# Performance work log

Hardware: AMD Instinct MI355X
Metric: run time of the kernel (lower is better)

Reference implementation:

```python
import jax, jax.numpy as jnp
import numpy as np

N_NODES = 100000
N_EDGES = 1600000
HIDDEN = 64
N_LAYERS = 3
N_CLASSES = 2
N_GRAPHS = 128
NEG_SLOPE = 0.2  # PyG GATConv default negative_slope


def setup_inputs() -> dict:
    key = jax.random.key(0)
    ks = jax.random.split(key, 8)
    x = jax.random.randint(ks[0], (N_NODES,), 0, 2)
    edge_index = jax.random.randint(ks[1], (2, N_EDGES), 0, N_NODES)
    batch = jnp.sort(jax.random.randint(ks[2], (N_NODES,), 0, N_GRAPHS))
    scale = 1.0 / np.sqrt(HIDDEN)
    embed_table = jax.random.normal(ks[3], (2, HIDDEN), jnp.float32)
    Ws = jax.random.normal(ks[4], (N_LAYERS, HIDDEN, HIDDEN), jnp.float32) * scale
    a_srcs = jax.random.normal(ks[5], (N_LAYERS, HIDDEN), jnp.float32) * scale
    a_dsts = jax.random.normal(ks[6], (N_LAYERS, HIDDEN), jnp.float32) * scale
    biases = jnp.zeros((N_LAYERS, HIDDEN), jnp.float32)
    W_out = jax.random.normal(ks[7], (HIDDEN, N_CLASSES), jnp.float32) * scale
    b_out = jnp.zeros((N_CLASSES,), jnp.float32)
    return {"x": x, "edge_index": edge_index, "batch": batch,
            "embed_table": embed_table, "Ws": Ws, "a_srcs": a_srcs,
            "a_dsts": a_dsts, "biases": biases, "W_out": W_out, "b_out": b_out}


def _gat_layer(h, src, dst, W, a_s, a_d, b):
    # h: [N, D]; src/dst: [E'] (self loops included) -> PyG GATConv, heads=1
    hW = h @ W                                   # [N, D]
    e = jax.nn.leaky_relu((hW @ a_s)[src] + (hW @ a_d)[dst], NEG_SLOPE)  # [E']
    m = jax.ops.segment_max(e, dst, num_segments=N_NODES)               # stable softmax per dst
    ex = jnp.exp(e - m[dst])
    denom = jax.ops.segment_sum(ex, dst, num_segments=N_NODES)
    alpha = ex / denom[dst]                      # [E']
    out = jax.ops.segment_sum(hW[src] * alpha[:, None], dst, num_segments=N_NODES)
    return out + b


def reference(x, edge_index, batch, embed_table, Ws, a_srcs, a_dsts, biases, W_out, b_out):
    loop = jnp.arange(N_NODES)
    src = jnp.concatenate([edge_index[0], loop])  # PyG add_self_loops=True
    dst = jnp.concatenate([edge_index[1], loop])
    h = embed_table[x]                            # [N, D]
    for l in range(N_LAYERS):
        h = _gat_layer(h, src, dst, Ws[l], a_srcs[l], a_dsts[l], biases[l])
        if l < N_LAYERS - 1:
            h = jax.nn.relu(h)
    sums = jax.ops.segment_sum(h, batch, num_segments=N_GRAPHS)
    counts = jax.ops.segment_sum(jnp.ones((N_NODES,), h.dtype), batch, num_segments=N_GRAPHS)
    pooled = sums / jnp.maximum(counts, 1.0)[:, None]  # global_mean_pool
    return pooled @ W_out + b_out                      # [G, num_classes]
```

## Files before the change

### kernel.cpp

```cpp
#include <hip/hip_runtime.h>
#include <hip/hip_bf16.h>
#include <float.h>

#define N_NODES 100000
#define N_EDGES 1600000
#define HIDDEN 64
#define N_GRAPHS 128
#define NEG_SLOPE 0.2f
#define ETOT (N_EDGES + N_NODES)

#define BSHIFT 9
#define NB ((N_NODES + 511) >> BSHIFT)
#define PAIR_CHUNK 4096
#define PAIR_BLOCKS ((N_EDGES + PAIR_CHUNK - 1) / PAIR_CHUNK)
#define XBIT_BLOCKS ((N_NODES + 255) / 256)
#define TBL_BLOCKS (NLVL / 4)
#define CAP 12288

#define NREP 64
#define REP_STRIDE 272
#define NLVL 512

__device__ __forceinline__ unsigned short f2bf(float f) {
    unsigned u = __float_as_uint(f);
    unsigned r = (u + 0x7FFFu + ((u >> 16) & 1u)) >> 16;
    return (unsigned short)r;
}
__device__ __forceinline__ float blo(unsigned u) { return __uint_as_float(u << 16); }
__device__ __forceinline__ float bhi(unsigned u) { return __uint_as_float(u & 0xFFFF0000u); }
__device__ __forceinline__ int sb0(unsigned u) { return (int)((unsigned)(u << 24)) >> 24; }
__device__ __forceinline__ int sb1(unsigned u) { return (int)((unsigned)(u << 16)) >> 24; }
__device__ __forceinline__ int sb2(unsigned u) { return (int)((unsigned)(u << 8)) >> 24; }
__device__ __forceinline__ int sb3(unsigned u) { return (int)u >> 24; }


__global__ __launch_bounds__(256) void k_prep(
    const int* __restrict__ x,
    const float* __restrict__ embed, const float* __restrict__ Ws,
    const float* __restrict__ biases, const float* __restrict__ a_srcs,
    const float* __restrict__ a_dsts, const float* __restrict__ W_out,
    int* __restrict__ gcnt, float* __restrict__ pool_acc,
    unsigned* __restrict__ xb,
    unsigned char* __restrict__ Tq8, float* __restrict__ Tscl,
    float* __restrict__ Ts1s, float* __restrict__ Ts1d,
    float* __restrict__ sparams)
{
    int t = threadIdx.x, b = blockIdx.x;

    if (b < TBL_BLOCKS) {
        if (b == 0 && t < NB) gcnt[t] = 0;
        if (b < NREP && t < 2 * N_GRAPHS) pool_acc[b * REP_STRIDE + t] = 0.f;

        int l = b * 4 + (t >> 6);
        int f = t & 63;
        float r0 = 0.f, r1 = 0.f;
#pragma unroll 8
        for (int k = 0; k < 64; ++k) {
            float w = Ws[k * 64 + f];
            r0 = fmaf(embed[k], w, r0);
            r1 = fmaf(embed[64 + k], w, r1);
        }
        if (l == 0) {
            float as = a_srcs[f], ad = a_dsts[f];
            float t0 = r0 * as, t1 = r1 * as, t2 = r0 * ad, t3 = r1 * ad;
#pragma unroll
            for (int off = 32; off >= 1; off >>= 1) {
                t0 += __shfl_xor(t0, off); t1 += __shfl_xor(t1, off);
                t2 += __shfl_xor(t2, off); t3 += __shfl_xor(t3, off);
            }
            if (f == 0) { sparams[0] = t0; sparams[1] = t1; sparams[2] = t2; sparams[3] = t3; }
        }
        if (l == 1) {
            float b2 = biases[128 + f];
            float t4 = b2 * W_out[f * 2];
            float t5 = b2 * W_out[f * 2 + 1];
#pragma unroll
            for (int off = 32; off >= 1; off >>= 1) {
                t4 += __shfl_xor(t4, off); t5 += __shfl_xor(t5, off);
            }
            if (f == 0) { sparams[4] = t4; sparams[5] = t5; }
        }
        float c1 = (float)l * (1.f / (NLVL - 1));
        float o = fmaxf(biases[f] + r0 + c1 * (r1 - r0), 0.f);
        const float* W1 = Ws + 4096;
        float h = 0.f;
#pragma unroll 8
        for (int k = 0; k < 64; ++k) h = fmaf(__shfl(o, k), W1[k * 64 + f], h);
        float ss = h * a_srcs[64 + f];
        float sd = h * a_dsts[64 + f];
        float am = fabsf(h);
#pragma unroll
        for (int off = 32; off >= 1; off >>= 1) {
            ss += __shfl_xor(ss, off);
            sd += __shfl_xor(sd, off);
            am = fmaxf(am, __shfl_xor(am, off));
        }
        float iscl = (am > 0.f) ? 127.f / am : 0.f;
        Tq8[l * 64 + f] = (unsigned char)(__float2int_rn(h * iscl) & 255);
        if (f == 0) { Tscl[l] = am * (1.f / 127.f); Ts1s[l] = ss; Ts1d[l] = sd; }
    } else {
        int i = (b - TBL_BLOCKS) * 256 + t;
        int lane = t & 63;
        bool bb = (i < N_NODES) && (x[i] != 0);
        unsigned long long m = __ballot(bb);
        int wid = i >> 6;
        if (i < N_NODES + 64) {
            if (lane == 0) xb[wid * 2] = (unsigned)m;
            if (lane == 32) xb[wid * 2 + 1] = (unsigned)(m >> 32);
        }
    }
}


__global__ __launch_bounds__(256) void k_scatter(
    const int* __restrict__ e0, const int* __restrict__ e1,
    const unsigned* __restrict__ xb, int* __restrict__ gcnt,
    int* __restrict__ pairs)
{
    __shared__ int hcnt[NB];
    __shared__ int base[NB];
    int t = threadIdx.x, b = blockIdx.x;
    if (t < NB) hcnt[t] = 0;
    __syncthreads();
    int ebase = b * PAIR_CHUNK;
    int ecount = min(PAIR_CHUNK, N_EDGES - ebase);
    for (int i = 4 * t; i < ecount; i += 1024) {
        int4 d4 = *(const int4*)(e1 + ebase + i);
        atomicAdd(&hcnt[d4.x >> BSHIFT], 1);
        atomicAdd(&hcnt[d4.y >> BSHIFT], 1);
        atomicAdd(&hcnt[d4.z >> BSHIFT], 1);
        atomicAdd(&hcnt[d4.w >> BSHIFT], 1);
    }
    __syncthreads();
    if (t < NB) {
        int c = hcnt[t];
        base[t] = c ? atomicAdd(&gcnt[t], c) : 0;
        hcnt[t] = 0;
    }
    __syncthreads();
    for (int i = 4 * t; i < ecount; i += 1024) {
        int4 s4 = *(const int4*)(e0 + ebase + i);
        int4 d4 = *(const int4*)(e1 + ebase + i);
        int ss[4] = {s4.x, s4.y, s4.z, s4.w};
        int dd[4] = {d4.x, d4.y, d4.z, d4.w};
#pragma unroll
        for (int j = 0; j < 4; ++j) {
            int s = ss[j], d = dd[j];
            int xv = (xb[s >> 5] >> (s & 31)) & 1;
            int B = d >> BSHIFT;
            int idx = atomicAdd(&hcnt[B], 1);
            pairs[B * CAP + base[B] + idx] = (xv << 26) | ((d & 511) << 17) | s;
        }
    }
}

__global__ __launch_bounds__(1024) void k_csr_bucket(
    const int* __restrict__ pairs, const int* __restrict__ gcnt,
    const int* __restrict__ x, const float* __restrict__ sparams,
    int* __restrict__ rowptr, int* __restrict__ col,
    unsigned short* __restrict__ cidx)
{
    __shared__ int deg[512];
    __shared__ int excl[512];
    __shared__ int cnt2[512];
    __shared__ int wsum[16];
    __shared__ int p0sh;
    int b = blockIdx.x;
    int t = threadIdx.x;
    int nb = b << BSHIFT;
    int nodes = min(512, N_NODES - nb);

    int pv = (t < b) ? gcnt[t] : 0;
#pragma unroll
    for (int off = 32; off >= 1; off >>= 1) pv += __shfl_xor(pv, off);
    if ((t & 63) == 0) wsum[t >> 6] = pv;
    __syncthreads();
    if (t == 0) {
        int s = 0;
#pragma unroll
        for (int i = 0; i < 16; ++i) s += wsum[i];
        p0sh = s;
    }

    int xself = 0;
    if (t < 512) {
        xself = (t < nodes) ? (x[nb + t] & 1) : 0;
        deg[t] = (t < nodes) ? (1 | (xself << 16)) : 0;
        cnt2[t] = 1;
    }
    __syncthreads();
    int cnt = gcnt[b];
    int pbase = b * CAP;
    for (int i = t; i < cnt; i += 1024) {
        int p = pairs[pbase + i];
        atomicAdd(&deg[(p >> 17) & 511], 1 | (((p >> 26) & 1) << 16));
    }
    __syncthreads();

    int packed = (t < 512) ? deg[t] : 0;
    int val = packed & 0xFFFF;
    int kx = packed >> 16;
    if (t < nodes) {
        float ss0 = sparams[0], ss1 = sparams[1];
        float sd = xself ? sparams[3] : sparams[2];
        float e0 = ss0 + sd; e0 = (e0 >= 0.f) ? e0 : NEG_SLOPE * e0;
        float e1 = ss1 + sd; e1 = (e1 >= 0.f) ? e1 : NEG_SLOPE * e1;
        float pp0 = __expf(e0), pp1 = __expf(e1);
        float kn = (float)kx, dn = (float)(val - kx);
        float c1 = kn * pp1 / (dn * pp0 + kn * pp1);
        cidx[nb + t] = (unsigned short)__float2int_rn(c1 * (float)(NLVL - 1));
    }

    int xx = val;
#pragma unroll
    for (int off = 1; off < 64; off <<= 1) {
        int y = __shfl_up(xx, off);
        if ((t & 63) >= off) xx += y;
    }
    if ((t & 63) == 63 && t < 512) wsum[t >> 6] = xx;
    __syncthreads();
    if (t == 0) {
        int s = 0;
#pragma unroll
        for (int i = 0; i < 8; ++i) { int v = wsum[i]; wsum[i] = s; s += v; }
    }
    __syncthreads();
    int ex = xx - val + wsum[t >> 6];
    if (t < 512) excl[t] = ex;

    int p0 = p0sh;
    int colbase = p0 + nb;
    if (t < nodes) {
        rowptr[nb + t] = colbase + ex;
        col[colbase + ex] = nb + t;
    }
    if (b == NB - 1 && t == 0) rowptr[N_NODES] = ETOT;
    __syncthreads();
    for (int i = t; i < cnt; i += 1024) {
        int p = pairs[pbase + i];
        int li = (p >> 17) & 511;
        int pos = colbase + excl[li] + atomicAdd(&cnt2[li], 1);
        col[pos] = p & 0x1FFFF;
    }
}


__global__ __launch_bounds__(256) void k_agg1(
    const unsigned char* __restrict__ Tq8, const float* __restrict__ Tscl,
    const float* __restrict__ Ts1s, const float* __restrict__ Ts1d,
    const unsigned short* __restrict__ cidx, const int* __restrict__ col,
    const int* __restrict__ rowptr, const float* __restrict__ bias,
    unsigned short* __restrict__ hout)
{
    __shared__ float2 stash[4][64];
    int t = threadIdx.x;
    int wave = t >> 6, lane = t & 63;
    int h = lane >> 5, hl = lane & 31;
    int base = blockIdx.x * 8 + wave * 2;
    if (base >= N_NODES) return;
    const char* hb = (const char*)Tq8;

    int node = base + h;
    bool valid = (node < N_NODES);
    int row = 0, end = 0;
    if (valid) { row = rowptr[node]; end = rowptr[node + 1]; }
    int deg = end - row;
    int degO = __shfl_xor(deg, 32);
    bool fast = (deg <= 32) && (degO <= 32);

    if (fast) {
        int idx = 0;
        float p = 0.f, sc = 0.f;
        if (hl < deg) idx = cidx[col[row + hl]];
        float sdi = Ts1d[__shfl(idx, h * 32)];
        if (hl < deg) {
            float ee = Ts1s[idx] + sdi;
            ee = (ee >= 0.f) ? ee : NEG_SLOPE * ee;
            p = __expf(ee);
            sc = Tscl[idx];
        }
        stash[wave][lane] = make_float2(p * sc, __int_as_float(idx * 64));

        int q = hl >> 4;
        int f = hl & 15;
        int f4 = f * 4;
        int sb = h * 32;
        float a0 = 0.f, a1 = 0.f, a2 = 0.f, a3 = 0.f;
        int degr = (deg + 7) & ~7;
        for (int j = q; j < degr; j += 8) {
            float2 e0 = stash[wave][sb + j];
            float2 e1 = stash[wave][sb + j + 2];
            float2 e2 = stash[wave][sb + j + 4];
            float2 e3 = stash[wave][sb + j + 6];
            unsigned v0 = *(const unsigned*)(hb + (__float_as_int(e0.y) + f4));
            unsigned v1 = *(const unsigned*)(hb + (__float_as_int(e1.y) + f4));
            unsigned v2 = *(const unsigned*)(hb + (__float_as_int(e2.y) + f4));
            unsigned v3 = *(const unsigned*)(hb + (__float_as_int(e3.y) + f4));
            a0 = fmaf(e0.x, (float)sb0(v0), a0);
            a1 = fmaf(e0.x, (float)sb1(v0), a1);
            a2 = fmaf(e0.x, (float)sb2(v0), a2);
            a3 = fmaf(e0.x, (float)sb3(v0), a3);
            a0 = fmaf(e1.x, (float)sb0(v1), a0);
            a1 = fmaf(e1.x, (float)sb1(v1), a1);
            a2 = fmaf(e1.x, (float)sb2(v1), a2);
            a3 = fmaf(e1.x, (float)sb3(v1), a3);
            a0 = fmaf(e2.x, (float)sb0(v2), a0);
            a1 = fmaf(e2.x, (float)sb1(v2), a1);
            a2 = fmaf(e2.x, (float)sb2(v2), a2);
            a3 = fmaf(e2.x, (float)sb3(v2), a3);
            a0 = fmaf(e3.x, (float)sb0(v3), a0);
            a1 = fmaf(e3.x, (float)sb1(v3), a1);
            a2 = fmaf(e3.x, (float)sb2(v3), a2);
            a3 = fmaf(e3.x, (float)sb3(v3), a3);
        }
        float denom = p;
#pragma unroll
        for (int off = 16; off >= 1; off >>= 1) denom += __shfl_xor(denom, off);
        float inv = 1.f / denom;
        a0 += __shfl_xor(a0, 16);
        a1 += __shfl_xor(a1, 16);
        a2 += __shfl_xor(a2, 16);
        a3 += __shfl_xor(a3, 16);
        if (hl < 16 && valid) {
            float4 bb = *(const float4*)&bias[4 * f];
            ushort4 pk;
            pk.x = f2bf(fmaxf(fmaf(a0, inv, bb.x), 0.f));
            pk.y = f2bf(fmaxf(fmaf(a1, inv, bb.y), 0.f));
            pk.z = f2bf(fmaxf(fmaf(a2, inv, bb.z), 0.f));
            pk.w = f2bf(fmaxf(fmaf(a3, inv, bb.w), 0.f));
            *(ushort4*)&hout[node * 64 + 4 * f] = pk;
        }
    } else {
        for (int s = 0; s < 2; ++s) {
            int nd = base + s;
            if (nd >= N_NODES) continue;
            int r = rowptr[nd], e = rowptr[nd + 1];
            float sdi = Ts1d[cidx[nd]];
            float m = -FLT_MAX;
            for (int j = r + lane; j < e; j += 64) {
                float ee = Ts1s[cidx[col[j]]] + sdi;
                ee = (ee >= 0.f) ? ee : NEG_SLOPE * ee;
                m = fmaxf(m, ee);
            }
#pragma unroll
            for (int off = 32; off >= 1; off >>= 1) m = fmaxf(m, __shfl_xor(m, off));
            float denom = 0.f;
            for (int j = r + lane; j < e; j += 64) {
                float ee = Ts1s[cidx[col[j]]] + sdi;
                ee = (ee >= 0.f) ? ee : NEG_SLOPE * ee;
                denom += __expf(ee - m);
            }
#pragma unroll
            for (int off = 32; off >= 1; off >>= 1) denom += __shfl_xor(denom, off);
            float inv = 1.f / denom;
            float acc = 0.f;
            for (int j = r; j < e; ++j) {
                int idxj = cidx[col[j]];
                float ee = Ts1s[idxj] + sdi;
                ee = (ee >= 0.f) ? ee : NEG_SLOPE * ee;
                float w = __expf(ee - m) * inv * Tscl[idxj];
                int bq = (int)(signed char)Tq8[idxj * 64 + lane];
                acc = fmaf(w, (float)bq, acc);
            }
            hout[nd * 64 + lane] = f2bf(fmaxf(acc + bias[lane], 0.f));
        }
    }
}


__global__ __launch_bounds__(256) void k_gemm2(
    const unsigned* __restrict__ h32, const float* __restrict__ W,
    const float* __restrict__ a_s, const float* __restrict__ a_d,
    const float* __restrict__ W_out,
    float2* __restrict__ z2, float* __restrict__ s_src, float* __restrict__ s_dst)
{
    __shared__ float Wl[64 * 64];
    __shared__ float hT[64 * 68];
    int t = threadIdx.x;
    int r0 = blockIdx.x * 64;

    for (int i = t; i < 4096; i += 256) Wl[i] = W[i];
    for (int i = t; i < 2048; i += 256) {
        int r = i >> 5, m = i & 31;
        int row = r0 + r;
        unsigned u = (row < N_NODES) ? h32[row * 32 + m] : 0u;
        hT[(2 * m) * 68 + r]     = blo(u);
        hT[(2 * m + 1) * 68 + r] = bhi(u);
    }
    __syncthreads();

    int tcol = t & 15;
    int trow = t >> 4;
    float acc[4][4];
#pragma unroll
    for (int i = 0; i < 4; ++i)
#pragma unroll
        for (int j = 0; j < 4; ++j) acc[i][j] = 0.f;

    for (int k = 0; k < 64; ++k) {
        float4 va = *(const float4*)&hT[k * 68 + trow * 4];
        float4 vb = *(const float4*)&Wl[k * 64 + tcol * 4];
        float a[4] = {va.x, va.y, va.z, va.w};
        float bb[4] = {vb.x, vb.y, vb.z, vb.w};
#pragma unroll
        for (int i = 0; i < 4; ++i)
#pragma unroll
            for (int j = 0; j < 4; ++j) acc[i][j] = fmaf(a[i], bb[j], acc[i][j]);
    }

    float4 as4 = *(const float4*)&a_s[tcol * 4];
    float4 ad4 = *(const float4*)&a_d[tcol * 4];
    float asr[4] = {as4.x, as4.y, as4.z, as4.w};
    float adr[4] = {ad4.x, ad4.y, ad4.z, ad4.w};
    float4 wa = *(const float4*)&W_out[8 * tcol];
    float4 wb = *(const float4*)&W_out[8 * tcol + 4];

#pragma unroll
    for (int i = 0; i < 4; ++i) {
        int row = r0 + trow * 4 + i;
        float ps = 0.f, pd = 0.f;
#pragma unroll
        for (int j = 0; j < 4; ++j) {
            ps = fmaf(acc[i][j], asr[j], ps);
            pd = fmaf(acc[i][j], adr[j], pd);
        }
        float z0 = acc[i][0] * wa.x + acc[i][1] * wa.z + acc[i][2] * wb.x + acc[i][3] * wb.z;
        float z1 = acc[i][0] * wa.y + acc[i][1] * wa.w + acc[i][2] * wb.y + acc[i][3] * wb.w;
#pragma unroll
        for (int off = 8; off >= 1; off >>= 1) {
            ps += __shfl_xor(ps, off);
            pd += __shfl_xor(pd, off);
            z0 += __shfl_xor(z0, off);
            z1 += __shfl_xor(z1, off);
        }
        if (row < N_NODES && tcol == 0) {
            s_src[row] = ps; s_dst[row] = pd;
            z2[row] = make_float2(z0, z1);
        }
    }
}


__global__ __launch_bounds__(256) void k_pool2(
    const float2* __restrict__ z2, const int* __restrict__ col,
    const int* __restrict__ rowptr, const float* __restrict__ s_src_in,
    const float* __restrict__ s_dst_in, const int* __restrict__ batch,
    float* __restrict__ pool_acc)
{
    int t = threadIdx.x;
    int wave = t >> 6, lane = t & 63;
    int h = lane >> 5, hl = lane & 31;
    int base0 = blockIdx.x * 32 + wave * 8;
    if (base0 >= N_NODES) return;
    float* rep = pool_acc + ((blockIdx.x * 4 + wave) & (NREP - 1)) * REP_STRIDE;

    int gcur = -1;
    float acc0 = 0.f, acc1 = 0.f;

#pragma unroll
    for (int i = 0; i < 4; ++i) {
        int node = base0 + 2 * i + h;
        bool valid = (node < N_NODES);
        int row = 0, end = 0;
        if (valid) { row = rowptr[node]; end = rowptr[node + 1]; }
        int deg = end - row;
        int degO = __shfl_xor(deg, 32);
        bool fast = (deg <= 32) && (degO <= 32);
        float r0 = 0.f, r1 = 0.f;

        if (fast) {
            float sdi = valid ? s_dst_in[node] : 0.f;
            float p = 0.f;
            float2 zv = make_float2(0.f, 0.f);
            if (hl < deg) {
                int c = col[row + hl];
                float ee = s_src_in[c] + sdi;
                ee = (ee >= 0.f) ? ee : NEG_SLOPE * ee;
                p = __expf(ee);
                zv = z2[c];
            }
            float n0 = p * zv.x, n1 = p * zv.y, dn = p;
#pragma unroll
            for (int off = 16; off >= 1; off >>= 1) {
                n0 += __shfl_xor(n0, off);
                n1 += __shfl_xor(n1, off);
                dn += __shfl_xor(dn, off);
            }
            float inv = 1.f / dn;
            r0 = n0 * inv; r1 = n1 * inv;
        } else {
            float rr0[2], rr1[2];
#pragma unroll
            for (int s = 0; s < 2; ++s) {
                rr0[s] = rr1[s] = 0.f;
                int nd = base0 + 2 * i + s;
                if (nd >= N_NODES) continue;
                int r = rowptr[nd], e = rowptr[nd + 1];
                float sdi = s_dst_in[nd];
                float n0 = 0.f, n1 = 0.f, dn = 0.f;
                for (int j = r + lane; j < e; j += 64) {
                    int c = col[j];
                    float ee = s_src_in[c] + sdi;
                    ee = (ee >= 0.f) ? ee : NEG_SLOPE * ee;
                    float p = __expf(ee);
                    float2 zv = z2[c];
                    n0 = fmaf(p, zv.x, n0);
                    n1 = fmaf(p, zv.y, n1);
                    dn += p;
                }
#pragma unroll
                for (int off = 32; off >= 1; off >>= 1) {
                    n0 += __shfl_xor(n0, off);
                    n1 += __shfl_xor(n1, off);
                    dn += __shfl_xor(dn, off);
                }
                float inv = 1.f / dn;
                rr0[s] = n0 * inv; rr1[s] = n1 * inv;
            }
            r0 = rr0[h]; r1 = rr1[h];
        }

        if (hl == 0 && valid) {
            int g = batch[node];
            if (g != gcur) {
                if (gcur >= 0) {
                    atomicAdd(&rep[gcur * 2], acc0);
                    atomicAdd(&rep[gcur * 2 + 1], acc1);
                }
                gcur = g; acc0 = r0; acc1 = r1;
            } else {
                acc0 += r0; acc1 += r1;
            }
        }
    }
    if (hl == 0 && gcur >= 0) {
        atomicAdd(&rep[gcur * 2], acc0);
        atomicAdd(&rep[gcur * 2 + 1], acc1);
    }
}


__device__ __forceinline__ int lower_bound_dev(const int* __restrict__ a, int n, int v) {
    int lo = 0, hi = n;
    while (lo < hi) {
        int mid = (lo + hi) >> 1;
        if (a[mid] < v) lo = mid + 1; else hi = mid;
    }
    return lo;
}

__global__ void k_head(const float* __restrict__ pool_acc,
                       const int* __restrict__ batch,
                       const float* __restrict__ b_out,
                       const float* __restrict__ sparams,
                       float* __restrict__ out)
{
    int t = threadIdx.x;
    if (t < 2 * N_GRAPHS) {
        float s = 0.f;
#pragma unroll 8
        for (int r = 0; r < NREP; ++r) s += pool_acc[r * REP_STRIDE + t];
        int g = t >> 1, c = t & 1;
        int start = lower_bound_dev(batch, N_NODES, g);
        int end = lower_bound_dev(batch, N_NODES, g + 1);
        float cnt = fmaxf((float)(end - start), 1.f);
        out[t] = s / cnt + sparams[4 + c] + b_out[c];
    }
}


extern "C" void kernel_launch(void* const* d_in, const int* in_sizes, int n_in,
                              void* d_out, int out_size, void* d_ws, size_t ws_size,
                              hipStream_t stream) {
    const int*   x       = (const int*)d_in[0];
    const int*   edge    = (const int*)d_in[1];
    const int*   batch   = (const int*)d_in[2];
    const float* embed   = (const float*)d_in[3];
    const float* Ws      = (const float*)d_in[4];
    const float* a_srcs  = (const float*)d_in[5];
    const float* a_dsts  = (const float*)d_in[6];
    const float* biases  = (const float*)d_in[7];
    const float* W_out   = (const float*)d_in[8];
    const float* b_out   = (const float*)d_in[9];
    float* out = (float*)d_out;

    char* ws = (char*)d_ws;
    size_t off = 0;
    auto alloc = [&](size_t bytes) -> void* {
        void* p = ws + off;
        off += (bytes + 255) & ~(size_t)255;
        return p;
    };
    unsigned short* hout  = (unsigned short*)alloc((size_t)N_NODES * 64 * sizeof(unsigned short));
    float2* z2      = (float2*)alloc((size_t)N_NODES * sizeof(float2));
    float* s_src0   = (float*)alloc((size_t)N_NODES * sizeof(float));
    float* s_dst0   = (float*)alloc((size_t)N_NODES * sizeof(float));
    unsigned short* cidx = (unsigned short*)alloc((size_t)N_NODES * sizeof(unsigned short));
    int*   rowptr   = (int*)alloc((size_t)(N_NODES + 1) * sizeof(int));
    int*   colA     = (int*)alloc((size_t)ETOT * sizeof(int));
    int*   gcnt     = (int*)alloc((size_t)NB * sizeof(int));
    float* pool_acc = (float*)alloc((size_t)(NREP * REP_STRIDE) * sizeof(float));
    unsigned* xb    = (unsigned*)alloc((size_t)3232 * sizeof(unsigned));
    unsigned char* Tq8 = (unsigned char*)alloc((size_t)NLVL * 64);
    float* Tscl     = (float*)alloc((size_t)NLVL * sizeof(float));
    float* Ts1s     = (float*)alloc((size_t)NLVL * sizeof(float));
    float* Ts1d     = (float*)alloc((size_t)NLVL * sizeof(float));
    float* sparams  = (float*)alloc((size_t)8 * sizeof(float));
    int*   pairs    = (int*)alloc((size_t)NB * CAP * sizeof(int));

    const int* e0 = edge;
    const int* e1 = edge + N_EDGES;

    k_prep<<<TBL_BLOCKS + XBIT_BLOCKS, 256, 0, stream>>>(
        x, embed, Ws, biases, a_srcs, a_dsts, W_out,
        gcnt, pool_acc, xb, Tq8, Tscl, Ts1s, Ts1d, sparams);
    k_scatter<<<PAIR_BLOCKS, 256, 0, stream>>>(e0, e1, xb, gcnt, pairs);
    k_csr_bucket<<<NB, 1024, 0, stream>>>(pairs, gcnt, x, sparams, rowptr, colA, cidx);

    k_agg1<<<(N_NODES + 7) / 8, 256, 0, stream>>>(
        Tq8, Tscl, Ts1s, Ts1d, cidx, colA, rowptr, biases + 64, hout);
    k_gemm2<<<(N_NODES + 63) / 64, 256, 0, stream>>>(
        (const unsigned*)hout, Ws + 8192, a_srcs + 128, a_dsts + 128, W_out,
        z2, s_src0, s_dst0);
    k_pool2<<<(N_NODES + 31) / 32, 256, 0, stream>>>(
        z2, colA, rowptr, s_src0, s_dst0, batch, pool_acc);
    k_head<<<1, 256, 0, stream>>>(pool_acc, batch, b_out, sparams, out);
}
```

Baseline: 211.6 us.

## Fuse layer-2 aggregation into GEMM, pack node scores, compute degrees with global atomics

Merges the layer-2 aggregation kernel and the following GEMM into one kernel. The aggregated rows now go straight into shared memory in fp32, so the bf16 intermediate buffer is never written to or read from global memory. Per-node attention scores and output projections are packed into one float4 array so the pooling kernel does a single gather per neighbour, and row pointers are staged in shared memory. Degree and x-count are now computed with global atomics during scatter rather than by a per-bucket shared pass, and the scatter chunk size is halved. The risks are heavy global atomic traffic on degx and lower occupancy from the larger shared-memory footprint of the fused kernel.

```diff
diff --git a/kernel.cpp b/kernel.cpp
--- a/kernel.cpp
+++ b/kernel.cpp
@@ -11,7 +11,7 @@
 
 #define BSHIFT 9
 #define NB ((N_NODES + 511) >> BSHIFT)
-#define PAIR_CHUNK 4096
+#define PAIR_CHUNK 2048
 #define PAIR_BLOCKS ((N_EDGES + PAIR_CHUNK - 1) / PAIR_CHUNK)
 #define XBIT_BLOCKS ((N_NODES + 255) / 256)
 #define TBL_BLOCKS (NLVL / 4)
@@ -26,8 +26,6 @@
     unsigned r = (u + 0x7FFFu + ((u >> 16) & 1u)) >> 16;
     return (unsigned short)r;
 }
-__device__ __forceinline__ float blo(unsigned u) { return __uint_as_float(u << 16); }
-__device__ __forceinline__ float bhi(unsigned u) { return __uint_as_float(u & 0xFFFF0000u); }
 __device__ __forceinline__ int sb0(unsigned u) { return (int)((unsigned)(u << 24)) >> 24; }
 __device__ __forceinline__ int sb1(unsigned u) { return (int)((unsigned)(u << 16)) >> 24; }
 __device__ __forceinline__ int sb2(unsigned u) { return (int)((unsigned)(u << 8)) >> 24; }
@@ -39,8 +37,8 @@
     const float* __restrict__ embed, const float* __restrict__ Ws,
     const float* __restrict__ biases, const float* __restrict__ a_srcs,
     const float* __restrict__ a_dsts, const float* __restrict__ W_out,
-    int* __restrict__ gcnt, float* __restrict__ pool_acc,
-    unsigned* __restrict__ xb,
+    int* __restrict__ gcnt, int* __restrict__ degx,
+    float* __restrict__ pool_acc, unsigned* __restrict__ xb,
     unsigned char* __restrict__ Tq8, float* __restrict__ Tscl,
     float* __restrict__ Ts1s, float* __restrict__ Ts1d,
     float* __restrict__ sparams)
@@ -100,6 +98,7 @@
         if (f == 0) { Tscl[l] = am * (1.f / 127.f); Ts1s[l] = ss; Ts1d[l] = sd; }
     } else {
         int i = (b - TBL_BLOCKS) * 256 + t;
+        if (i < N_NODES) degx[i] = 0;
         int lane = t & 63;
         bool bb = (i < N_NODES) && (x[i] != 0);
         unsigned long long m = __ballot(bb);
@@ -115,7 +114,7 @@
 __global__ __launch_bounds__(256) void k_scatter(
     const int* __restrict__ e0, const int* __restrict__ e1,
     const unsigned* __restrict__ xb, int* __restrict__ gcnt,
-    int* __restrict__ pairs)
+    int* __restrict__ degx, int* __restrict__ pairs)
 {
     __shared__ int hcnt[NB];
     __shared__ int base[NB];
@@ -147,20 +146,21 @@
         for (int j = 0; j < 4; ++j) {
             int s = ss[j], d = dd[j];
             int xv = (xb[s >> 5] >> (s & 31)) & 1;
+            atomicAdd(&degx[d], 1 | (xv << 16));
             int B = d >> BSHIFT;
             int idx = atomicAdd(&hcnt[B], 1);
-            pairs[B * CAP + base[B] + idx] = (xv << 26) | ((d & 511) << 17) | s;
+            pairs[B * CAP + base[B] + idx] = ((d & 511) << 17) | s;
         }
     }
 }
 
 __global__ __launch_bounds__(1024) void k_csr_bucket(
     const int* __restrict__ pairs, const int* __restrict__ gcnt,
-    const int* __restrict__ x, const float* __restrict__ sparams,
+    const int* __restrict__ degx, const int* __restrict__ x,
+    const float* __restrict__ sparams,
     int* __restrict__ rowptr, int* __restrict__ col,
     unsigned short* __restrict__ cidx)
 {
-    __shared__ int deg[512];
     __shared__ int excl[512];
     __shared__ int cnt2[512];
     __shared__ int wsum[16];
@@ -181,26 +181,15 @@
         for (int i = 0; i < 16; ++i) s += wsum[i];
         p0sh = s;
     }
-
-    int xself = 0;
-    if (t < 512) {
-        xself = (t < nodes) ? (x[nb + t] & 1) : 0;
-        deg[t] = (t < nodes) ? (1 | (xself << 16)) : 0;
-        cnt2[t] = 1;
-    }
-    __syncthreads();
-    int cnt = gcnt[b];
-    int pbase = b * CAP;
-    for (int i = t; i < cnt; i += 1024) {
-        int p = pairs[pbase + i];
-        atomicAdd(&deg[(p >> 17) & 511], 1 | (((p >> 26) & 1) << 16));
-    }
-    __syncthreads();
-
-    int packed = (t < 512) ? deg[t] : 0;
-    int val = packed & 0xFFFF;
-    int kx = packed >> 16;
+    __syncthreads();
+
+    int val = 0, kx = 0;
+    if (t < 512) cnt2[t] = 1;
     if (t < nodes) {
+        int xself = x[nb + t] & 1;
+        int dx = degx[nb + t];
+        val = (dx & 0xFFFF) + 1;
+        kx = (dx >> 16) + xself;
         float ss0 = sparams[0], ss1 = sparams[1];
         float sd = xself ? sparams[3] : sparams[2];
         float e0 = ss0 + sd; e0 = (e0 >= 0.f) ? e0 : NEG_SLOPE * e0;
@@ -236,6 +225,8 @@
     }
     if (b == NB - 1 && t == 0) rowptr[N_NODES] = ETOT;
     __syncthreads();
+    int cnt = gcnt[b];
+    int pbase = b * CAP;
     for (int i = t; i < cnt; i += 1024) {
         int p = pairs[pbase + i];
         int li = (p >> 17) & 511;
@@ -245,147 +236,137 @@
 }
 
 
-__global__ __launch_bounds__(256) void k_agg1(
+__global__ __launch_bounds__(256) void k_l2(
     const unsigned char* __restrict__ Tq8, const float* __restrict__ Tscl,
     const float* __restrict__ Ts1s, const float* __restrict__ Ts1d,
     const unsigned short* __restrict__ cidx, const int* __restrict__ col,
     const int* __restrict__ rowptr, const float* __restrict__ bias,
-    unsigned short* __restrict__ hout)
+    const float* __restrict__ W, const float* __restrict__ a_s,
+    const float* __restrict__ a_d, const float* __restrict__ W_out,
+    float4* __restrict__ szz)
 {
+    __shared__ float Wl[64 * 64];
+    __shared__ float hT[64 * 68];
     __shared__ float2 stash[4][64];
+    __shared__ int rp[65];
     int t = threadIdx.x;
     int wave = t >> 6, lane = t & 63;
     int h = lane >> 5, hl = lane & 31;
-    int base = blockIdx.x * 8 + wave * 2;
-    if (base >= N_NODES) return;
+    int r0 = blockIdx.x * 64;
     const char* hb = (const char*)Tq8;
 
-    int node = base + h;
-    bool valid = (node < N_NODES);
-    int row = 0, end = 0;
-    if (valid) { row = rowptr[node]; end = rowptr[node + 1]; }
-    int deg = end - row;
-    int degO = __shfl_xor(deg, 32);
-    bool fast = (deg <= 32) && (degO <= 32);
-
-    if (fast) {
-        int idx = 0;
-        float p = 0.f, sc = 0.f;
-        if (hl < deg) idx = cidx[col[row + hl]];
-        float sdi = Ts1d[__shfl(idx, h * 32)];
-        if (hl < deg) {
-            float ee = Ts1s[idx] + sdi;
-            ee = (ee >= 0.f) ? ee : NEG_SLOPE * ee;
-            p = __expf(ee);
-            sc = Tscl[idx];
-        }
-        stash[wave][lane] = make_float2(p * sc, __int_as_float(idx * 64));
-
-        int q = hl >> 4;
-        int f = hl & 15;
-        int f4 = f * 4;
-        int sb = h * 32;
-        float a0 = 0.f, a1 = 0.f, a2 = 0.f, a3 = 0.f;
-        int degr = (deg + 7) & ~7;
-        for (int j = q; j < degr; j += 8) {
-            float2 e0 = stash[wave][sb + j];
-            float2 e1 = stash[wave][sb + j + 2];
-            float2 e2 = stash[wave][sb + j + 4];
-            float2 e3 = stash[wave][sb + j + 6];
-            unsigned v0 = *(const unsigned*)(hb + (__float_as_int(e0.y) + f4));
-            unsigned v1 = *(const unsigned*)(hb + (__float_as_int(e1.y) + f4));
-            unsigned v2 = *(const unsigned*)(hb + (__float_as_int(e2.y) + f4));
-            unsigned v3 = *(const unsigned*)(hb + (__float_as_int(e3.y) + f4));
-            a0 = fmaf(e0.x, (float)sb0(v0), a0);
-            a1 = fmaf(e0.x, (float)sb1(v0), a1);
-            a2 = fmaf(e0.x, (float)sb2(v0), a2);
-            a3 = fmaf(e0.x, (float)sb3(v0), a3);
-            a0 = fmaf(e1.x, (float)sb0(v1), a0);
-            a1 = fmaf(e1.x, (float)sb1(v1), a1);
-            a2 = fmaf(e1.x, (float)sb2(v1), a2);
-            a3 = fmaf(e1.x, (float)sb3(v1), a3);
-            a0 = fmaf(e2.x, (float)sb0(v2), a0);
-            a1 = fmaf(e2.x, (float)sb1(v2), a1);
-            a2 = fmaf(e2.x, (float)sb2(v2), a2);
-            a3 = fmaf(e2.x, (float)sb3(v2), a3);
-            a0 = fmaf(e3.x, (float)sb0(v3), a0);
-            a1 = fmaf(e3.x, (float)sb1(v3), a1);
-            a2 = fmaf(e3.x, (float)sb2(v3), a2);
-            a3 = fmaf(e3.x, (float)sb3(v3), a3);
-        }
-        float denom = p;
-#pragma unroll
-        for (int off = 16; off >= 1; off >>= 1) denom += __shfl_xor(denom, off);
-        float inv = 1.f / denom;
-        a0 += __shfl_xor(a0, 16);
-        a1 += __shfl_xor(a1, 16);
-        a2 += __shfl_xor(a2, 16);
-        a3 += __shfl_xor(a3, 16);
-        if (hl < 16 && valid) {
-            float4 bb = *(const float4*)&bias[4 * f];
-            ushort4 pk;
-            pk.x = f2bf(fmaxf(fmaf(a0, inv, bb.x), 0.f));
-            pk.y = f2bf(fmaxf(fmaf(a1, inv, bb.y), 0.f));
-            pk.z = f2bf(fmaxf(fmaf(a2, inv, bb.z), 0.f));
-            pk.w = f2bf(fmaxf(fmaf(a3, inv, bb.w), 0.f));
-            *(ushort4*)&hout[node * 64 + 4 * f] = pk;
-        }
-    } else {
-        for (int s = 0; s < 2; ++s) {
-            int nd = base + s;
-            if (nd >= N_NODES) continue;
-            int r = rowptr[nd], e = rowptr[nd + 1];
-            float sdi = Ts1d[cidx[nd]];
-            float m = -FLT_MAX;
-            for (int j = r + lane; j < e; j += 64) {
-                float ee = Ts1s[cidx[col[j]]] + sdi;
+    for (int i = t; i < 4096; i += 256) Wl[i] = W[i];
+    if (t < 65) {
+        int n = r0 + t;
+        rp[t] = (n <= N_NODES) ? rowptr[n] : ETOT;
+    }
+    __syncthreads();
+
+    for (int rr = 0; rr < 8; ++rr) {
+        int nl = rr * 8 + wave * 2 + h;
+        bool valid = (r0 + nl < N_NODES);
+        int row = valid ? rp[nl] : 0;
+        int end = valid ? rp[nl + 1] : 0;
+        int deg = end - row;
+        int degO = __shfl_xor(deg, 32);
+        bool fast = (deg <= 32) && (degO <= 32);
+
+        if (fast) {
+            int idx = 0;
+            float p = 0.f, sc = 0.f;
+            if (hl < deg) idx = cidx[col[row + hl]];
+            float sdi = Ts1d[__shfl(idx, h * 32)];
+            if (hl < deg) {
+                float ee = Ts1s[idx] + sdi;
                 ee = (ee >= 0.f) ? ee : NEG_SLOPE * ee;
-                m = fmaxf(m, ee);
-            }
-#pragma unroll
-            for (int off = 32; off >= 1; off >>= 1) m = fmaxf(m, __shfl_xor(m, off));
-            float denom = 0.f;
-            for (int j = r + lane; j < e; j += 64) {
-                float ee = Ts1s[cidx[col[j]]] + sdi;
-                ee = (ee >= 0.f) ? ee : NEG_SLOPE * ee;
-                denom += __expf(ee - m);
-            }
-#pragma unroll
-            for (int off = 32; off >= 1; off >>= 1) denom += __shfl_xor(denom, off);
+                p = __expf(ee);
+                sc = Tscl[idx];
+            }
+            stash[wave][lane] = make_float2(p * sc, __int_as_float(idx * 64));
+
+            int q = hl >> 4;
+            int f = hl & 15;
+            int f4 = f * 4;
+            int sb = h * 32;
+            float a0 = 0.f, a1 = 0.f, a2 = 0.f, a3 = 0.f;
+            int degr = (deg + 7) & ~7;
+            for (int j = q; j < degr; j += 8) {
+                float2 e0 = stash[wave][sb + j];
+                float2 e1 = stash[wave][sb + j + 2];
+                float2 e2 = stash[wave][sb + j + 4];
+                float2 e3 = stash[wave][sb + j + 6];
+                unsigned v0 = *(const unsigned*)(hb + (__float_as_int(e0.y) + f4));
+                unsigned v1 = *(const unsigned*)(hb + (__float_as_int(e1.y) + f4));
+                unsigned v2 = *(const unsigned*)(hb + (__float_as_int(e2.y) + f4));
+                unsigned v3 = *(const unsigned*)(hb + (__float_as_int(e3.y) + f4));
+                a0 = fmaf(e0.x, (float)sb0(v0), a0);
+                a1 = fmaf(e0.x, (float)sb1(v0), a1);
+                a2 = fmaf(e0.x, (float)sb2(v0), a2);
+                a3 = fmaf(e0.x, (float)sb3(v0), a3);
+                a0 = fmaf(e1.x, (float)sb0(v1), a0);
+                a1 = fmaf(e1.x, (float)sb1(v1), a1);
+                a2 = fmaf(e1.x, (float)sb2(v1), a2);
+                a3 = fmaf(e1.x, (float)sb3(v1), a3);
+                a0 = fmaf(e2.x, (float)sb0(v2), a0);
+                a1 = fmaf(e2.x, (float)sb1(v2), a1);
+                a2 = fmaf(e2.x, (float)sb2(v2), a2);
+                a3 = fmaf(e2.x, (float)sb3(v2), a3);
+                a0 = fmaf(e3.x, (float)sb0(v3), a0);
+                a1 = fmaf(e3.x, (float)sb1(v3), a1);
+                a2 = fmaf(e3.x, (float)sb2(v3), a2);
+                a3 = fmaf(e3.x, (float)sb3(v3), a3);
+            }
+            float denom = p;
+#pragma unroll
+            for (int off = 16; off >= 1; off >>= 1) denom += __shfl_xor(denom, off);
             float inv = 1.f / denom;
-            float acc = 0.f;
-            for (int j = r; j < e; ++j) {
-                int idxj = cidx[col[j]];
-                float ee = Ts1s[idxj] + sdi;
-                ee = (ee >= 0.f) ? ee : NEG_SLOPE * ee;
-                float w = __expf(ee - m) * inv * Tscl[idxj];
-                int bq = (int)(signed char)Tq8[idxj * 64 + lane];
-                acc = fmaf(w, (float)bq, acc);
-            }
-            hout[nd * 64 + lane] = f2bf(fmaxf(acc + bias[lane], 0.f));
-        }
-    }
-}
-
-
-__global__ __launch_bounds__(256) void k_gemm2(
-    const unsigned* __restrict__ h32, const float* __restrict__ W,
-    const float* __restrict__ a_s, const float* __restrict__ a_d,
-    const float* __restrict__ W_out,
-    float2* __restrict__ z2, float* __restrict__ s_src, float* __restrict__ s_dst)
-{
-    __shared__ float Wl[64 * 64];
-    __shared__ float hT[64 * 68];
-    int t = threadIdx.x;
-    int r0 = blockIdx.x * 64;
-
-    for (int i = t; i < 4096; i += 256) Wl[i] = W[i];
-    for (int i = t; i < 2048; i += 256) {
-        int r = i >> 5, m = i & 31;
-        int row = r0 + r;
-        unsigned u = (row < N_NODES) ? h32[row * 32 + m] : 0u;
-        hT[(2 * m) * 68 + r]     = blo(u);
-        hT[(2 * m + 1) * 68 + r] = bhi(u);
+            a0 += __shfl_xor(a0, 16);
+            a1 += __shfl_xor(a1, 16);
+            a2 += __shfl_xor(a2, 16);
+            a3 += __shfl_xor(a3, 16);
+            if (hl < 16 && valid) {
+                float4 bb4 = *(const float4*)&bias[4 * f];
+                hT[(4 * f + 0) * 68 + nl] = fmaxf(fmaf(a0, inv, bb4.x), 0.f);
+                hT[(4 * f + 1) * 68 + nl] = fmaxf(fmaf(a1, inv, bb4.y), 0.f);
+                hT[(4 * f + 2) * 68 + nl] = fmaxf(fmaf(a2, inv, bb4.z), 0.f);
+                hT[(4 * f + 3) * 68 + nl] = fmaxf(fmaf(a3, inv, bb4.w), 0.f);
+            }
+        } else {
+            for (int s = 0; s < 2; ++s) {
+                int nls = rr * 8 + wave * 2 + s;
+                int nd = r0 + nls;
+                if (nd >= N_NODES) continue;
+                int r = rp[nls], e = rp[nls + 1];
+                float sdi = Ts1d[cidx[nd]];
+                float m = -FLT_MAX;
+                for (int j = r + lane; j < e; j += 64) {
+                    float ee = Ts1s[cidx[col[j]]] + sdi;
+                    ee = (ee >= 0.f) ? ee : NEG_SLOPE * ee;
+                    m = fmaxf(m, ee);
+                }
+#pragma unroll
+                for (int off = 32; off >= 1; off >>= 1) m = fmaxf(m, __shfl_xor(m, off));
+                float denom = 0.f;
+                for (int j = r + lane; j < e; j += 64) {
+                    float ee = Ts1s[cidx[col[j]]] + sdi;
+                    ee = (ee >= 0.f) ? ee : NEG_SLOPE * ee;
+                    denom += __expf(ee - m);
+                }
+#pragma unroll
+                for (int off = 32; off >= 1; off >>= 1) denom += __shfl_xor(denom, off);
+                float inv = 1.f / denom;
+                float acc = 0.f;
+                for (int j = r; j < e; ++j) {
+                    int idxj = cidx[col[j]];
+                    float ee = Ts1s[idxj] + sdi;
+                    ee = (ee >= 0.f) ? ee : NEG_SLOPE * ee;
+                    float w = __expf(ee - m) * inv * Tscl[idxj];
+                    int bq = (int)(signed char)Tq8[idxj * 64 + lane];
+                    acc = fmaf(w, (float)bq, acc);
+                }
+                hT[lane * 68 + nls] = fmaxf(acc + bias[lane], 0.f);
+            }
+        }
     }
     __syncthreads();
 
@@ -417,7 +398,7 @@
 
 #pragma unroll
     for (int i = 0; i < 4; ++i) {
-        int row = r0 + trow * 4 + i;
+        int orow = r0 + trow * 4 + i;
         float ps = 0.f, pd = 0.f;
 #pragma unroll
         for (int j = 0; j < 4; ++j) {
@@ -433,25 +414,28 @@
             z0 += __shfl_xor(z0, off);
             z1 += __shfl_xor(z1, off);
         }
-        if (row < N_NODES && tcol == 0) {
-            s_src[row] = ps; s_dst[row] = pd;
-            z2[row] = make_float2(z0, z1);
+        if (orow < N_NODES && tcol == 0) {
+            szz[orow] = make_float4(ps, z0, z1, pd);
         }
     }
 }
 
 
 __global__ __launch_bounds__(256) void k_pool2(
-    const float2* __restrict__ z2, const int* __restrict__ col,
-    const int* __restrict__ rowptr, const float* __restrict__ s_src_in,
-    const float* __restrict__ s_dst_in, const int* __restrict__ batch,
+    const float4* __restrict__ szz, const int* __restrict__ col,
+    const int* __restrict__ rowptr, const int* __restrict__ batch,
     float* __restrict__ pool_acc)
 {
+    __shared__ int rp2[33];
     int t = threadIdx.x;
     int wave = t >> 6, lane = t & 63;
     int h = lane >> 5, hl = lane & 31;
-    int base0 = blockIdx.x * 32 + wave * 8;
-    if (base0 >= N_NODES) return;
+    int nb0 = blockIdx.x * 32;
+    if (t < 33) {
+        int n = nb0 + t;
+        rp2[t] = (n <= N_NODES) ? rowptr[n] : ETOT;
+    }
+    __syncthreads();
     float* rep = pool_acc + ((blockIdx.x * 4 + wave) & (NREP - 1)) * REP_STRIDE;
 
     int gcur = -1;
@@ -459,27 +443,28 @@
 
 #pragma unroll
     for (int i = 0; i < 4; ++i) {
-        int node = base0 + 2 * i + h;
+        int nls = wave * 8 + 2 * i + h;
+        int node = nb0 + nls;
         bool valid = (node < N_NODES);
-        int row = 0, end = 0;
-        if (valid) { row = rowptr[node]; end = rowptr[node + 1]; }
+        int row = valid ? rp2[nls] : 0;
+        int end = valid ? rp2[nls + 1] : 0;
         int deg = end - row;
         int degO = __shfl_xor(deg, 32);
         bool fast = (deg <= 32) && (degO <= 32);
         float r0 = 0.f, r1 = 0.f;
 
         if (fast) {
-            float sdi = valid ? s_dst_in[node] : 0.f;
-            float p = 0.f;
-            float2 zv = make_float2(0.f, 0.f);
+            float sdi = valid ? szz[node].w : 0.f;
+            float p = 0.f, zy = 0.f, zz = 0.f;
             if (hl < deg) {
                 int c = col[row + hl];
-                float ee = s_src_in[c] + sdi;
+                float4 sz = szz[c];
+                float ee = sz.x + sdi;
                 ee = (ee >= 0.f) ? ee : NEG_SLOPE * ee;
                 p = __expf(ee);
-                zv = z2[c];
-            }
-            float n0 = p * zv.x, n1 = p * zv.y, dn = p;
+                zy = sz.y; zz = sz.z;
+            }
+            float n0 = p * zy, n1 = p * zz, dn = p;
 #pragma unroll
             for (int off = 16; off >= 1; off >>= 1) {
                 n0 += __shfl_xor(n0, off);
@@ -493,19 +478,20 @@
 #pragma unroll
             for (int s = 0; s < 2; ++s) {
                 rr0[s] = rr1[s] = 0.f;
-                int nd = base0 + 2 * i + s;
+                int nds = wave * 8 + 2 * i + s;
+                int nd = nb0 + nds;
                 if (nd >= N_NODES) continue;
-                int r = rowptr[nd], e = rowptr[nd + 1];
-                float sdi = s_dst_in[nd];
+                int r = rp2[nds], e = rp2[nds + 1];
+                float sdi = szz[nd].w;
                 float n0 = 0.f, n1 = 0.f, dn = 0.f;
                 for (int j = r + lane; j < e; j += 64) {
                     int c = col[j];
-                    float ee = s_src_in[c] + sdi;
+                    float4 sz = szz[c];
+                    float ee = sz.x + sdi;
                     ee = (ee >= 0.f) ? ee : NEG_SLOPE * ee;
                     float p = __expf(ee);
-                    float2 zv = z2[c];
-                    n0 = fmaf(p, zv.x, n0);
-                    n1 = fmaf(p, zv.y, n1);
+                    n0 = fmaf(p, sz.y, n0);
+                    n1 = fmaf(p, sz.z, n1);
                     dn += p;
                 }
 #pragma unroll
@@ -591,14 +577,12 @@
         off += (bytes + 255) & ~(size_t)255;
         return p;
     };
-    unsigned short* hout  = (unsigned short*)alloc((size_t)N_NODES * 64 * sizeof(unsigned short));
-    float2* z2      = (float2*)alloc((size_t)N_NODES * sizeof(float2));
-    float* s_src0   = (float*)alloc((size_t)N_NODES * sizeof(float));
-    float* s_dst0   = (float*)alloc((size_t)N_NODES * sizeof(float));
+    float4* szz     = (float4*)alloc((size_t)N_NODES * sizeof(float4));
     unsigned short* cidx = (unsigned short*)alloc((size_t)N_NODES * sizeof(unsigned short));
     int*   rowptr   = (int*)alloc((size_t)(N_NODES + 1) * sizeof(int));
     int*   colA     = (int*)alloc((size_t)ETOT * sizeof(int));
     int*   gcnt     = (int*)alloc((size_t)NB * sizeof(int));
+    int*   degx     = (int*)alloc((size_t)N_NODES * sizeof(int));
     float* pool_acc = (float*)alloc((size_t)(NREP * REP_STRIDE) * sizeof(float));
     unsigned* xb    = (unsigned*)alloc((size_t)3232 * sizeof(unsigned));
     unsigned char* Tq8 = (unsigned char*)alloc((size_t)NLVL * 64);
@@ -613,16 +597,13 @@
 
     k_prep<<<TBL_BLOCKS + XBIT_BLOCKS, 256, 0, stream>>>(
         x, embed, Ws, biases, a_srcs, a_dsts, W_out,
-        gcnt, pool_acc, xb, Tq8, Tscl, Ts1s, Ts1d, sparams);
-    k_scatter<<<PAIR_BLOCKS, 256, 0, stream>>>(e0, e1, xb, gcnt, pairs);
-    k_csr_bucket<<<NB, 1024, 0, stream>>>(pairs, gcnt, x, sparams, rowptr, colA, cidx);
-
-    k_agg1<<<(N_NODES + 7) / 8, 256, 0, stream>>>(
-        Tq8, Tscl, Ts1s, Ts1d, cidx, colA, rowptr, biases + 64, hout);
-    k_gemm2<<<(N_NODES + 63) / 64, 256, 0, stream>>>(
-        (const unsigned*)hout, Ws + 8192, a_srcs + 128, a_dsts + 128, W_out,
-        z2, s_src0, s_dst0);
+        gcnt, degx, pool_acc, xb, Tq8, Tscl, Ts1s, Ts1d, sparams);
+    k_scatter<<<PAIR_BLOCKS, 256, 0, stream>>>(e0, e1, xb, gcnt, degx, pairs);
+    k_csr_bucket<<<NB, 1024, 0, stream>>>(pairs, gcnt, degx, x, sparams, rowptr, colA, cidx);
+    k_l2<<<(N_NODES + 63) / 64, 256, 0, stream>>>(
+        Tq8, Tscl, Ts1s, Ts1d, cidx, colA, rowptr, biases + 64,
+        Ws + 8192, a_srcs + 128, a_dsts + 128, W_out, szz);
     k_pool2<<<(N_NODES + 31) / 32, 256, 0, stream>>>(
-        z2, colA, rowptr, s_src0, s_dst0, batch, pool_acc);
+        szz, colA, rowptr, batch, pool_acc);
     k_head<<<1, 256, 0, stream>>>(pool_acc, batch, b_out, sparams, out);
 }
```

After: 275.0 us. 1.3x slower.
